# Performance work log

Measured on AMD Instinct MI355X. Metric: run time of the kernel, lower is better.

Reference implementation:

```python
import math
import jax, jax.numpy as jnp
import numpy as np

NQ = 4   # n_qubits
NL = 2   # n_layers
H = 16   # num_heads


def _apply_gate(state, gate, q, batched):
    """Apply a 1-qubit gate on wire q to batched state [N, 2**NQ]."""
    n = state.shape[0]
    left, right = 2 ** q, 2 ** (NQ - 1 - q)
    s = state.reshape(n, left, 2, right)
    eq = 'nab,nlbr->nlar' if batched else 'ab,nlbr->nlar'
    return jnp.einsum(eq, gate, s).reshape(n, 2 ** NQ)


def _rot(phi, theta, omega):
    """PennyLane Rot(phi, theta, omega) = RZ(omega) RY(theta) RZ(phi), 2x2 unitary."""
    c = jnp.cos(theta / 2).astype(jnp.complex64)
    s = jnp.sin(theta / 2).astype(jnp.complex64)
    ep = jnp.exp(-0.5j * (phi + omega).astype(jnp.complex64))
    em = jnp.exp(0.5j * (phi - omega).astype(jnp.complex64))
    m00 = ep * c
    m01 = -em * s
    m10 = jnp.conj(em) * s
    m11 = jnp.conj(ep) * c
    return jnp.stack([jnp.stack([m00, m01]), jnp.stack([m10, m11])])


def _cnot01(state):
    """CNOT with control wire 0, target wire 1 on [N, 16]."""
    n = state.shape[0]
    s = state.reshape(n, 2, 2, 2 ** (NQ - 2))
    s = jnp.stack([s[:, 0], s[:, 1, ::-1]], axis=1)
    return s.reshape(n, 2 ** NQ)


def _quantum_block(inputs, params):
    """Analytic state-vector simulation of the PennyLane circuit.

    inputs: [N, NQ] rotation angles (AngleEmbedding, default RX).
    params: [NL, NQ, 3] Rot parameters.
    Returns [N, NQ] Pauli-Z expectation values.
    """
    n = inputs.shape[0]
    state = jnp.zeros((n, 2 ** NQ), jnp.complex64).at[:, 0].set(1.0)
    # AngleEmbedding: RX(inputs[:, q]) on wire q
    for q in range(NQ):
        a = inputs[:, q] * 0.5
        c = jnp.cos(a).astype(jnp.complex64)
        s = (-1j) * jnp.sin(a).astype(jnp.complex64)
        gate = jnp.stack([jnp.stack([c, s], -1), jnp.stack([s, c], -1)], -2)  # [N,2,2]
        state = _apply_gate(state, gate, q, batched=True)
    # Variational layers
    for l in range(NL):
        for q in range(NQ):
            g = _rot(params[l, q, 0], params[l, q, 1], params[l, q, 2])
            state = _apply_gate(state, g, q, batched=False)
        state = _cnot01(state)
    probs = (jnp.abs(state) ** 2).reshape(n, 2, 2, 2, 2)
    z = jnp.array([1.0, -1.0], probs.dtype)
    letters = 'abcd'
    evs = [jnp.einsum(f'nabcd,{letters[i]}->n', probs, z) for i in range(NQ)]
    return jnp.stack(evs, axis=-1)


def reference(x, params, w_q, w_k, w_v, w_o):
    B, S, E = x.shape
    dk = E // H

    def proj(w):
        return (x @ w.T).reshape(B, S, H, dk).transpose(0, 2, 1, 3)  # [B,H,S,dk]

    q, k, v = proj(w_q), proj(w_k), proj(w_v)

    def inject(t):
        ang = t[..., :NQ].reshape(-1, NQ)
        ev = _quantum_block(ang, params).reshape(B, H, S, NQ).astype(t.dtype)
        return t.at[..., :NQ].set(ev)

    q, k, v = inject(q), inject(k), inject(v)
    scores = jnp.einsum('bhqd,bhkd->bhqk', q, k) / math.sqrt(dk)
    attn = jax.nn.softmax(scores, axis=-1)
    out = jnp.einsum('bhqk,bhkd->bhqd', attn, v)
    out = out.transpose(0, 2, 1, 3).reshape(B, S, E)
    return out @ w_o.T


def setup_inputs() -> dict:
    key = jax.random.key(0)
    ks = jax.random.split(key, 6)
    B, S, E = 2, 2048, 1024
    scale = 1.0 / math.sqrt(E)
    return {
        'x': jax.random.normal(ks[0], (B, S, E), jnp.float32),
        'params': jax.random.normal(ks[1], (NL, NQ, 3), jnp.float32),
        'w_q': jax.random.normal(ks[2], (E, E), jnp.float32) * scale,
        'w_k': jax.random.normal(ks[3], (E, E), jnp.float32) * scale,
        'w_v': jax.random.normal(ks[4], (E, E), jnp.float32) * scale,
        'w_o': jax.random.normal(ks[5], (E, E), jnp.float32) * scale,
    }
```

## Files before the change

### kernel.cpp

```cpp
#include <hip/hip_runtime.h>
#include <math.h>

#define BATCH 2
#define S_LEN 2048
#define E_DIM 1024
#define NHEAD 16
#define DK 64
#define NROWS (BATCH * S_LEN)

typedef _Float16 f16x8 __attribute__((ext_vector_type(8)));
typedef _Float16 f16x4 __attribute__((ext_vector_type(4)));
typedef float    f32x4 __attribute__((ext_vector_type(4)));

__device__ __forceinline__ void glds16(_Float16* lds, const _Float16* g) {
    __builtin_amdgcn_global_load_lds(
        (const __attribute__((address_space(1))) unsigned int*)g,
        (__attribute__((address_space(3))) unsigned int*)lds,
        16, 0, 0);
}

__global__ __launch_bounds__(256) void conv_all(
    const float* __restrict__ x,  const float* __restrict__ wq,
    const float* __restrict__ wk, const float* __restrict__ wv,
    const float* __restrict__ wo,
    _Float16* __restrict__ xh,  _Float16* __restrict__ wqh,
    _Float16* __restrict__ wkh, _Float16* __restrict__ wvh,
    _Float16* __restrict__ woh) {
    const int id = blockIdx.x;
    const float* src; _Float16* dst; int lid;
    if (id < 4096)      { src = x;  dst = xh;  lid = id; }
    else if (id < 5120) { src = wq; dst = wqh; lid = id - 4096; }
    else if (id < 6144) { src = wk; dst = wkh; lid = id - 5120; }
    else if (id < 7168) { src = wv; dst = wvh; lid = id - 6144; }
    else                { src = wo; dst = woh; lid = id - 7168; }
    const int i = lid * 256 + threadIdx.x;
    float4 v = ((const float4*)src)[i];
    f16x4 h;
    h[0] = (_Float16)v.x; h[1] = (_Float16)v.y;
    h[2] = (_Float16)v.z; h[3] = (_Float16)v.w;
    ((f16x4*)dst)[i] = h;
}

__device__ __forceinline__ void gemm_body(const _Float16* __restrict__ X,
                                          const _Float16* __restrict__ W,
                                          void* __restrict__ dstv, int mode,
                                          _Float16* smem) {
    _Float16* Xs = smem;
    _Float16* Ws = smem + 128 * 64;

    const int tid  = threadIdx.x;
    const int lane = tid & 63;
    const int w    = tid >> 6;
    const int wy = w >> 1, wx = w & 1;
    const int l15 = lane & 15, quad = lane >> 4;
    const int sw  = l15 & 7;
    const int m0 = blockIdx.y * 128, c0 = blockIdx.x * 128;

    const int lrow = lane >> 3;
    const int gcol = ((lane & 7) ^ lrow) * 8;
    const _Float16* xg = X + (size_t)(m0 + w * 32 + lrow) * E_DIM + gcol;
    const _Float16* wg = W + (size_t)(c0 + w * 32 + lrow) * E_DIM + gcol;
    _Float16* xls = Xs + (w * 32) * 64;
    _Float16* wls = Ws + (w * 32) * 64;

    f32x4 acc[4][4];
#pragma unroll
    for (int i = 0; i < 4; ++i)
#pragma unroll
        for (int j = 0; j < 4; ++j) acc[i][j] = 0.f;

    for (int k0 = 0; k0 < E_DIM; k0 += 64) {
        __syncthreads();
#pragma unroll
        for (int c = 0; c < 4; ++c)
            glds16(xls + c * 512, xg + (size_t)c * 8 * E_DIM + k0);
#pragma unroll
        for (int c = 0; c < 4; ++c)
            glds16(wls + c * 512, wg + (size_t)c * 8 * E_DIM + k0);
        __syncthreads();

#pragma unroll
        for (int ks = 0; ks < 2; ++ks) {
            f16x8 af[4], bf[4];
#pragma unroll
            for (int i = 0; i < 4; ++i) {
                const int pc = ((ks * 4 + quad) ^ sw) * 8;
                af[i] = *(const f16x8*)&Xs[(wy * 64 + i * 16 + l15) * 64 + pc];
                bf[i] = *(const f16x8*)&Ws[(wx * 64 + i * 16 + l15) * 64 + pc];
            }
#pragma unroll
            for (int i = 0; i < 4; ++i)
#pragma unroll
                for (int j = 0; j < 4; ++j)
                    acc[i][j] = __builtin_amdgcn_mfma_f32_16x16x32_f16(af[i], bf[j], acc[i][j], 0, 0, 0);
        }
    }

    if (mode == 2) {
        __syncthreads();
        _Float16* Ct = smem;
#pragma unroll
        for (int i = 0; i < 4; ++i)
#pragma unroll
            for (int j = 0; j < 4; ++j) {
                const int col  = wx * 64 + j * 16 + l15;
                const int rowb = wy * 64 + i * 16 + quad * 4;
                f16x4 pk;
#pragma unroll
                for (int r = 0; r < 4; ++r) pk[r] = (_Float16)acc[i][j][r];
                *(f16x4*)&Ct[col * 136 + rowb] = pk;
            }
        __syncthreads();
        const int b  = m0 >> 11;
        const int s0 = m0 & 2047;
#pragma unroll
        for (int it = 0; it < 8; ++it) {
            const int c   = it * 256 + tid;
            const int col = c >> 4;
            const int rc  = c & 15;
            f16x8 v = *(const f16x8*)&Ct[col * 136 + rc * 8];
            const int e = c0 + col, h = e >> 6, d = e & 63;
            *(f16x8*)((_Float16*)dstv + ((size_t)((b * NHEAD + h) * DK + d)) * S_LEN + s0 + rc * 8) = v;
        }
        return;
    }

#pragma unroll
    for (int i = 0; i < 4; ++i)
#pragma unroll
        for (int j = 0; j < 4; ++j)
#pragma unroll
            for (int r = 0; r < 4; ++r) {
                const int row = m0 + wy * 64 + i * 16 + quad * 4 + r;
                const int col = c0 + wx * 64 + j * 16 + l15;
                if (mode == 0) {
                    ((float*)dstv)[(size_t)row * E_DIM + col] = acc[i][j][r];
                } else {
                    const int b = row >> 11, s = row & 2047;
                    const int h = col >> 6,  d = col & 63;
                    ((_Float16*)dstv)[(((size_t)(b * NHEAD + h) * S_LEN + s) * DK) + d] =
                        (_Float16)acc[i][j][r];
                }
            }
}

__global__ __launch_bounds__(256, 3) void gemm_qkv(
    const _Float16* __restrict__ X,
    const _Float16* __restrict__ WQ, const _Float16* __restrict__ WK,
    const _Float16* __restrict__ WV,
    _Float16* __restrict__ Qh, _Float16* __restrict__ Kh,
    _Float16* __restrict__ VTh) {
    __shared__ __align__(16) _Float16 smem[128 * 136];
    const int z = blockIdx.z;
    const _Float16* W = (z == 0) ? WQ : (z == 1) ? WK : WV;
    void* dst = (z == 0) ? (void*)Qh : (z == 1) ? (void*)Kh : (void*)VTh;
    gemm_body(X, W, dst, (z == 2) ? 2 : 1, smem);
}

__global__ __launch_bounds__(256, 3) void gemm_out(const _Float16* __restrict__ X,
                                                   const _Float16* __restrict__ W,
                                                   float* __restrict__ dst) {
    __shared__ __align__(16) _Float16 smem[128 * 136];
    gemm_body(X, W, dst, 0, smem);
}

__device__ __forceinline__ void apply_gate(float ar[16], float ai[16], int stride,
                                           float g00r, float g00i, float g01r, float g01i,
                                           float g10r, float g10i, float g11r, float g11i) {
#pragma unroll
    for (int i0 = 0; i0 < 16; ++i0) {
        if (i0 & stride) continue;
        const int i1 = i0 + stride;
        const float s0r = ar[i0], s0i = ai[i0];
        const float s1r = ar[i1], s1i = ai[i1];
        ar[i0] = g00r * s0r - g00i * s0i + g01r * s1r - g01i * s1i;
        ai[i0] = g00r * s0i + g00i * s0r + g01r * s1i + g01i * s1r;
        ar[i1] = g10r * s0r - g10i * s0i + g11r * s1r - g11i * s1i;
        ai[i1] = g10r * s0i + g10i * s0r + g11r * s1i + g11i * s1r;
    }
}

__global__ __launch_bounds__(256) void quantum_inject(_Float16* __restrict__ Q,
                                                      _Float16* __restrict__ K,
                                                      _Float16* __restrict__ VT,
                                                      const float* __restrict__ params) {
    const int id = blockIdx.x * 256 + threadIdx.x;
    const int which = id >> 16;
    const int rem = id & 65535;

    float angv[4];
    _Float16* qkbase = nullptr;
    _Float16* vbase  = nullptr;
    if (which == 2) {
        const int bh = rem >> 11, s = rem & 2047;
        vbase = VT + ((size_t)bh * DK) * S_LEN + s;
#pragma unroll
        for (int d = 0; d < 4; ++d) angv[d] = (float)vbase[(size_t)d * S_LEN];
    } else {
        qkbase = (which == 0 ? Q : K) + (size_t)rem * DK;
        const f16x4 a4 = *(const f16x4*)qkbase;
#pragma unroll
        for (int d = 0; d < 4; ++d) angv[d] = (float)a4[d];
    }

    float ar[16], ai[16];
#pragma unroll
    for (int i = 0; i < 16; ++i) { ar[i] = 0.f; ai[i] = 0.f; }
    ar[0] = 1.f;

#pragma unroll
    for (int q = 0; q < 4; ++q) {
        float sh, ch;
        sincosf(0.5f * angv[q], &sh, &ch);
        apply_gate(ar, ai, 8 >> q, ch, 0.f, 0.f, -sh, 0.f, -sh, ch, 0.f);
    }

#pragma unroll
    for (int l = 0; l < 2; ++l) {
#pragma unroll
        for (int q = 0; q < 4; ++q) {
            const float* pp = params + (l * 4 + q) * 3;
            const float phi = pp[0], th = pp[1], om = pp[2];
            float st, ct, sa, ca, sb, cb;
            sincosf(0.5f * th, &st, &ct);
            sincosf(0.5f * (phi + om), &sa, &ca);
            sincosf(0.5f * (phi - om), &sb, &cb);
            apply_gate(ar, ai, 8 >> q,
                       ct * ca, -ct * sa,
                       -st * cb, -st * sb,
                       st * cb, -st * sb,
                       ct * ca, ct * sa);
        }
#pragma unroll
        for (int r = 0; r < 4; ++r) {
            float tr = ar[8 + r], ti = ai[8 + r];
            ar[8 + r] = ar[12 + r]; ai[8 + r] = ai[12 + r];
            ar[12 + r] = tr;        ai[12 + r] = ti;
        }
    }

    float ev[4] = {0.f, 0.f, 0.f, 0.f};
#pragma unroll
    for (int i = 0; i < 16; ++i) {
        const float p = ar[i] * ar[i] + ai[i] * ai[i];
        ev[0] += (i & 8) ? -p : p;
        ev[1] += (i & 4) ? -p : p;
        ev[2] += (i & 2) ? -p : p;
        ev[3] += (i & 1) ? -p : p;
    }
    if (which == 2) {
#pragma unroll
        for (int d = 0; d < 4; ++d) vbase[(size_t)d * S_LEN] = (_Float16)ev[d];
    } else {
        f16x4 o;
#pragma unroll
        for (int d = 0; d < 4; ++d) o[d] = (_Float16)ev[d];
        *(f16x4*)qkbase = o;
    }
}

__global__ __launch_bounds__(256, 3) void attn7(const _Float16* __restrict__ Q,
                                                const _Float16* __restrict__ K,
                                                const _Float16* __restrict__ VT,
                                                _Float16* __restrict__ ctx) {
    __shared__ __align__(16) _Float16 KVs[2][2][64 * 64];

    const int tid = threadIdx.x, lane = tid & 63, w = tid >> 6;
    const int l15 = lane & 15, quad = lane >> 4;
    const int sw  = l15 & 7;
    const int bh = blockIdx.y;
    const int qbase = blockIdx.x * 128 + w * 32;

    const _Float16* Qb = Q  + (size_t)bh * S_LEN * DK;
    const _Float16* Kb = K  + (size_t)bh * S_LEN * DK;
    const _Float16* Vb = VT + (size_t)bh * DK * S_LEN;

    const int lrow = lane >> 3;
    const int gcol = ((lane & 7) ^ lrow) * 8;
    const int sr0  = 32 * (w >> 1) + 8 * (lrow >> 2) + 4 * (w & 1) + (lrow & 3);
    const _Float16* kg = Kb + (size_t)sr0 * DK + gcol;
    const _Float16* vg = Vb + (size_t)(w * 16 + lrow) * S_LEN + gcol;

    f16x8 bf[2][2];
#pragma unroll
    for (int qn = 0; qn < 2; ++qn)
#pragma unroll
        for (int ks = 0; ks < 2; ++ks)
            bf[qn][ks] = *(const f16x8*)(Qb + (size_t)(qbase + qn * 16 + l15) * DK + ks * 32 + quad * 8);

    f32x4 oacc[4][2];
#pragma unroll
    for (int dt = 0; dt < 4; ++dt)
#pragma unroll
        for (int qn = 0; qn < 2; ++qn) oacc[dt][qn] = 0.f;
    float lpart[2] = {0.f, 0.f};

#pragma unroll
    for (int c = 0; c < 2; ++c) {
        glds16(&KVs[0][0][(w * 16 + c * 8) * 64], kg + (size_t)(c * 16) * DK);
        glds16(&KVs[0][1][(w * 16 + c * 8) * 64], vg + (size_t)(c * 8) * S_LEN);
    }
    __syncthreads();

    for (int t = 0; t < S_LEN / 64; ++t) {
        const int buf = t & 1;
        if (t < S_LEN / 64 - 1) {
            const int kt = (t + 1) * 64;
#pragma unroll
            for (int c = 0; c < 2; ++c) {
                glds16(&KVs[buf ^ 1][0][(w * 16 + c * 8) * 64],
                       kg + (size_t)(kt + c * 16) * DK);
                glds16(&KVs[buf ^ 1][1][(w * 16 + c * 8) * 64],
                       vg + (size_t)(c * 8) * S_LEN + kt);
            }
        }

        f16x8 af[4][2], vt[4][2];
#pragma unroll
        for (int kc = 0; kc < 4; ++kc)
#pragma unroll
            for (int ks = 0; ks < 2; ++ks)
                af[kc][ks] = *(const f16x8*)&KVs[buf][0][(kc * 16 + l15) * 64 + ((ks * 4 + quad) ^ sw) * 8];
#pragma unroll
        for (int dt = 0; dt < 4; ++dt)
#pragma unroll
            for (int kh = 0; kh < 2; ++kh)
                vt[dt][kh] = *(const f16x8*)&KVs[buf][1][(dt * 16 + l15) * 64 + ((kh * 4 + quad) ^ sw) * 8];

        f16x4 pk4s[4][2];
#pragma unroll
        for (int kc = 0; kc < 4; ++kc)
#pragma unroll
            for (int qn = 0; qn < 2; ++qn) {
                f32x4 st = 0.f;
                st = __builtin_amdgcn_mfma_f32_16x16x32_f16(af[kc][0], bf[qn][0], st, 0, 0, 0);
                st = __builtin_amdgcn_mfma_f32_16x16x32_f16(af[kc][1], bf[qn][1], st, 0, 0, 0);
                float ps = 0.f;
                f16x4 pk;
#pragma unroll
                for (int r = 0; r < 4; ++r) {
                    const float p = __builtin_amdgcn_exp2f(
                        fmaf(st[r], 0.18033688011f, -4.32808512267f));
                    ps += p;
                    pk[r] = (_Float16)p;
                }
                lpart[qn] += ps;
                pk4s[kc][qn] = pk;
            }

#pragma unroll
        for (int dt = 0; dt < 4; ++dt)
#pragma unroll
            for (int qn = 0; qn < 2; ++qn)
#pragma unroll
                for (int kh = 0; kh < 2; ++kh) {
                    const f16x8 pb = __builtin_shufflevector(
                        pk4s[2 * kh][qn], pk4s[2 * kh + 1][qn],
                        0, 1, 2, 3, 4, 5, 6, 7);
                    oacc[dt][qn] = __builtin_amdgcn_mfma_f32_16x16x32_f16(
                        vt[dt][kh], pb, oacc[dt][qn], 0, 0, 0);
                }

        __syncthreads();
    }

    float inv[2];
#pragma unroll
    for (int qn = 0; qn < 2; ++qn) {
        float l = lpart[qn];
        l += __shfl_xor(l, 16);
        l += __shfl_xor(l, 32);
        inv[qn] = 1.f / l;
    }

    _Float16* ep = &KVs[0][0][0] + w * (32 * 72);
#pragma unroll
    for (int dt = 0; dt < 4; ++dt)
#pragma unroll
        for (int qn = 0; qn < 2; ++qn) {
            f16x4 ov;
#pragma unroll
            for (int r = 0; r < 4; ++r) ov[r] = (_Float16)(oacc[dt][qn][r] * inv[qn]);
            *(f16x4*)&ep[(qn * 16 + l15) * 72 + dt * 16 + quad * 4] = ov;
        }

    const int b = bh >> 4, h = bh & 15;
#pragma unroll
    for (int i = 0; i < 4; ++i) {
        const int c = i * 64 + lane;
        const int row = c >> 3, c8 = c & 7;
        f16x8 v = *(const f16x8*)&ep[row * 72 + c8 * 8];
        *(f16x8*)(ctx + (size_t)(b * S_LEN + qbase + row) * E_DIM + h * DK + c8 * 8) = v;
    }
}

extern "C" void kernel_launch(void* const* d_in, const int* in_sizes, int n_in,
                              void* d_out, int out_size, void* d_ws, size_t ws_size,
                              hipStream_t stream) {
    const float* x      = (const float*)d_in[0];
    const float* params = (const float*)d_in[1];
    const float* w_q    = (const float*)d_in[2];
    const float* w_k    = (const float*)d_in[3];
    const float* w_v    = (const float*)d_in[4];
    const float* w_o    = (const float*)d_in[5];
    float* out = (float*)d_out;

    const size_t TENS = (size_t)NROWS * E_DIM;
    const size_t WEL  = (size_t)E_DIM * E_DIM;
    _Float16* xh  = (_Float16*)d_ws;
    _Float16* wqh = xh  + TENS;
    _Float16* wkh = wqh + WEL;
    _Float16* wvh = wkh + WEL;
    _Float16* woh = wvh + WEL;
    _Float16* Qh  = woh + WEL;
    _Float16* Kh  = Qh  + TENS;
    _Float16* VTh = Kh  + TENS;
    _Float16* CTXh= VTh + TENS;

    dim3 blk(256);

    conv_all<<<dim3(8192), blk, 0, stream>>>(x, w_q, w_k, w_v, w_o,
                                             xh, wqh, wkh, wvh, woh);

    gemm_qkv<<<dim3(E_DIM / 128, NROWS / 128, 3), blk, 0, stream>>>(
        xh, wqh, wkh, wvh, Qh, Kh, VTh);

    quantum_inject<<<dim3(768), blk, 0, stream>>>(Qh, Kh, VTh, params);

    attn7<<<dim3(S_LEN / 128, BATCH * NHEAD), blk, 0, stream>>>(Qh, Kh, VTh, CTXh);

    gemm_out<<<dim3(E_DIM / 128, NROWS / 128), blk, 0, stream>>>(CTXh, woh, out);
}
```

Measured before the change: 198.3 us.

## Split attention over two key halves with a separate combine kernel

The attention kernel now splits the key/value sequence into two halves along a new grid z dimension, doubling the number of blocks. Each block writes unnormalized fp32 partial outputs and row sums to workspace, and a new combine kernel adds the halves, normalizes and writes fp16 context. Launch bounds are raised to target 4 blocks per CU. This is meant to improve CU fill and occupancy. In exchange it adds fp32 partial-result traffic, an extra launch, and a risk of register pressure under the tighter bounds.

New measurement: 208.6 us. 5.2% more time.

```diff
diff --git a/kernel.cpp b/kernel.cpp
--- a/kernel.cpp
+++ b/kernel.cpp
@@ -259,16 +259,19 @@
     }
 }
 
-__global__ __launch_bounds__(256, 3) void attn7(const _Float16* __restrict__ Q,
+__global__ __launch_bounds__(256, 4) void attn9(const _Float16* __restrict__ Q,
                                                 const _Float16* __restrict__ K,
                                                 const _Float16* __restrict__ VT,
-                                                _Float16* __restrict__ ctx) {
+                                                float* __restrict__ Opart,
+                                                float* __restrict__ Lpart) {
     __shared__ __align__(16) _Float16 KVs[2][2][64 * 64];
 
     const int tid = threadIdx.x, lane = tid & 63, w = tid >> 6;
     const int l15 = lane & 15, quad = lane >> 4;
     const int sw  = l15 & 7;
     const int bh = blockIdx.y;
+    const int z  = blockIdx.z;
+    const int kt0 = z * (S_LEN / 2);
     const int qbase = blockIdx.x * 128 + w * 32;
 
     const _Float16* Qb = Q  + (size_t)bh * S_LEN * DK;
@@ -297,15 +300,15 @@
 
 #pragma unroll
     for (int c = 0; c < 2; ++c) {
-        glds16(&KVs[0][0][(w * 16 + c * 8) * 64], kg + (size_t)(c * 16) * DK);
-        glds16(&KVs[0][1][(w * 16 + c * 8) * 64], vg + (size_t)(c * 8) * S_LEN);
+        glds16(&KVs[0][0][(w * 16 + c * 8) * 64], kg + (size_t)(kt0 + c * 16) * DK);
+        glds16(&KVs[0][1][(w * 16 + c * 8) * 64], vg + (size_t)(c * 8) * S_LEN + kt0);
     }
     __syncthreads();
 
-    for (int t = 0; t < S_LEN / 64; ++t) {
+    for (int t = 0; t < S_LEN / 128; ++t) {
         const int buf = t & 1;
-        if (t < S_LEN / 64 - 1) {
-            const int kt = (t + 1) * 64;
+        if (t < S_LEN / 128 - 1) {
+            const int kt = kt0 + (t + 1) * 64;
 #pragma unroll
             for (int c = 0; c < 2; ++c) {
                 glds16(&KVs[buf ^ 1][0][(w * 16 + c * 8) * 64],
@@ -364,34 +367,46 @@
         __syncthreads();
     }
 
-    float inv[2];
+    const size_t rowbase = ((size_t)(z * 32 + bh)) * S_LEN + qbase;
 #pragma unroll
     for (int qn = 0; qn < 2; ++qn) {
         float l = lpart[qn];
         l += __shfl_xor(l, 16);
         l += __shfl_xor(l, 32);
-        inv[qn] = 1.f / l;
-    }
-
-    _Float16* ep = &KVs[0][0][0] + w * (32 * 72);
+        if (quad == 0) Lpart[rowbase + qn * 16 + l15] = l;
+    }
 #pragma unroll
     for (int dt = 0; dt < 4; ++dt)
 #pragma unroll
-        for (int qn = 0; qn < 2; ++qn) {
-            f16x4 ov;
-#pragma unroll
-            for (int r = 0; r < 4; ++r) ov[r] = (_Float16)(oacc[dt][qn][r] * inv[qn]);
-            *(f16x4*)&ep[(qn * 16 + l15) * 72 + dt * 16 + quad * 4] = ov;
-        }
-
+        for (int qn = 0; qn < 2; ++qn)
+            *(f32x4*)&Opart[(rowbase + qn * 16 + l15) * DK + dt * 16 + quad * 4] =
+                oacc[dt][qn];
+}
+
+__global__ __launch_bounds__(256) void attn_combine(const float* __restrict__ Opart,
+                                                    const float* __restrict__ Lpart,
+                                                    _Float16* __restrict__ ctx) {
+    const int t  = blockIdx.x * 256 + threadIdx.x;
+    const int qi = t >> 3;
+    const int dc = (t & 7) * 8;
+    const float l   = Lpart[qi] + Lpart[65536 + qi];
+    const float inv = 1.f / l;
+    const float4 a0 = *(const float4*)&Opart[(size_t)qi * DK + dc];
+    const float4 a1 = *(const float4*)&Opart[(size_t)qi * DK + dc + 4];
+    const float4 b0 = *(const float4*)&Opart[(size_t)(65536 + qi) * DK + dc];
+    const float4 b1 = *(const float4*)&Opart[(size_t)(65536 + qi) * DK + dc + 4];
+    f16x8 o;
+    o[0] = (_Float16)((a0.x + b0.x) * inv);
+    o[1] = (_Float16)((a0.y + b0.y) * inv);
+    o[2] = (_Float16)((a0.z + b0.z) * inv);
+    o[3] = (_Float16)((a0.w + b0.w) * inv);
+    o[4] = (_Float16)((a1.x + b1.x) * inv);
+    o[5] = (_Float16)((a1.y + b1.y) * inv);
+    o[6] = (_Float16)((a1.z + b1.z) * inv);
+    o[7] = (_Float16)((a1.w + b1.w) * inv);
+    const int bh = qi >> 11, s = qi & 2047;
     const int b = bh >> 4, h = bh & 15;
-#pragma unroll
-    for (int i = 0; i < 4; ++i) {
-        const int c = i * 64 + lane;
-        const int row = c >> 3, c8 = c & 7;
-        f16x8 v = *(const f16x8*)&ep[row * 72 + c8 * 8];
-        *(f16x8*)(ctx + (size_t)(b * S_LEN + qbase + row) * E_DIM + h * DK + c8 * 8) = v;
-    }
+    *(f16x8*)(ctx + ((size_t)(b * S_LEN + s)) * E_DIM + h * DK + dc) = o;
 }
 
 extern "C" void kernel_launch(void* const* d_in, const int* in_sizes, int n_in,
@@ -416,6 +431,8 @@
     _Float16* Kh  = Qh  + TENS;
     _Float16* VTh = Kh  + TENS;
     _Float16* CTXh= VTh + TENS;
+    float* Opart  = (float*)(CTXh + TENS);
+    float* Lpart  = Opart + (size_t)2 * 65536 * DK;
 
     dim3 blk(256);
 
@@ -427,7 +444,10 @@
 
     quantum_inject<<<dim3(768), blk, 0, stream>>>(Qh, Kh, VTh, params);
 
-    attn7<<<dim3(S_LEN / 128, BATCH * NHEAD), blk, 0, stream>>>(Qh, Kh, VTh, CTXh);
+    attn9<<<dim3(S_LEN / 128, BATCH * NHEAD, 2), blk, 0, stream>>>(
+        Qh, Kh, VTh, Opart, Lpart);
+
+    attn_combine<<<dim3(2048), blk, 0, stream>>>(Opart, Lpart, CTXh);
 
     gemm_out<<<dim3(E_DIM / 128, NROWS / 128), blk, 0, stream>>>(CTXh, woh, out);
 }
```
